# Kernel optimization log

Measured on AMD Instinct MI355X. Metric: run time of the kernel, lower is better.

Reference implementation:

```python
import jax, jax.numpy as jnp
import numpy as np

# Module config (matches init_kwargs)
H, W, C = 32, 32, 256
K = 3                      # filter_size
B = 16
TEMP = 1.0                 # softmax_temp
CH, CW = H - K + 1, W - K + 1   # convs_height/width (valid padding, stride 1)
NF = CH * CW               # num_convs
FS = K * K                 # filter_size squared (window size)
HW = H * W


def _local_indices():
    # flattened (row-major over H,W) positions of each KxK window, sorted ascending
    idx = np.zeros((NF, FS), dtype=np.int32)
    c = 0
    for i in range(CH):
        for j in range(CW):
            win = [(i + di) * W + (j + dj) for di in range(K) for dj in range(K)]
            idx[c] = np.sort(win)
            c += 1
    return jnp.asarray(idx)


def setup_inputs() -> dict:
    key = jax.random.key(0)
    ks = jax.random.split(key, 7)
    s = 1.0 / np.sqrt(C)  # torch Linear default init scale
    return {
        "batch": jax.random.normal(ks[0], (B, C, H, W), dtype=jnp.float32),
        "key_w": jax.random.uniform(ks[1], (C, C), jnp.float32, -s, s),
        "key_b": jax.random.uniform(ks[2], (C,), jnp.float32, -s, s),
        "query_w": jax.random.uniform(ks[3], (C, C), jnp.float32, -s, s),
        "query_b": jax.random.uniform(ks[4], (C,), jnp.float32, -s, s),
        "value_w": jax.random.uniform(ks[5], (1, C), jnp.float32, -s, s),
        "value_b": jax.random.uniform(ks[6], (1,), jnp.float32, -s, s),
        "local_indices": _local_indices(),
    }


def _normalize(t):
    # F.normalize(dim=-1), eps=1e-12
    return t / jnp.maximum(jnp.linalg.norm(t, axis=-1, keepdims=True), 1e-12)


def reference(batch, key_w, key_b, query_w, query_b, value_w, value_b, local_indices):
    # [B,C,H,W] -> [B,HW,C]
    x = batch.transpose(0, 2, 3, 1).reshape(B, HW, C)
    # local patches: X_l[f,b,k,c] = x[b, local_indices[f,k], c]  -> [NF,B,FS,C]
    X_l = x[:, local_indices].transpose(1, 0, 2, 3)
    # global is the full (unmasked) feature map: X_g = x  -> [B,HW,C]
    keys = x @ key_w.T + key_b                       # [B,HW,C]
    queries = X_l @ query_w.T + query_b              # [NF,B,FS,C]
    values = (x @ value_w.T + value_b)[..., 0]       # [B,HW]
    # cosine similarity: [NF,B,HW,FS]
    comp = jnp.einsum('bnc,fbkc->fbnk', _normalize(keys), _normalize(queries))
    att = jax.nn.softmax(TEMP * comp, axis=2)        # softmax over HW
    # W_g[f,b,k] = sum_n values[b,n] * att[f,b,n,k]
    W_g = jnp.einsum('bn,fbnk->fbk', values, att)
    # convolved: sum over window positions, weighted
    conv = jnp.einsum('fbk,fbkc->fbc', W_g, X_l)     # [NF,B,C]
    out = conv.transpose(1, 0, 2).reshape(B, CH, CW, C).transpose(0, 3, 1, 2)
    return out  # [B,C,CH,CW]
```

## Files before the change

kernel.cpp:

```cpp
#include <hip/hip_runtime.h>
#include <hip/hip_bf16.h>


#define NB 16
#define NC 256
#define NHW 1024
#define NCH 30

typedef __attribute__((ext_vector_type(8))) short short8;
typedef __attribute__((ext_vector_type(4))) float f32x4;

static __device__ __forceinline__ unsigned short f2bf(float f) {
    __hip_bfloat16 h = __float2bfloat16(f);
    return *(unsigned short*)&h;
}
static __device__ __forceinline__ float bf2f(unsigned short u) {
    unsigned int x = ((unsigned int)u) << 16;
    return __uint_as_float(x);
}

__global__ __launch_bounds__(256) void wconv_kernel(
    const float* __restrict__ key_w, const float* __restrict__ query_w,
    unsigned short* __restrict__ kpk, unsigned short* __restrict__ qpk)
{
    const int gx = blockIdx.x;
    const int mat = gx >> 3, g = gx & 7, t = threadIdx.x;
    const float* src = mat ? query_w : key_w;
    unsigned short* dst = mat ? qpk : kpk;
    #pragma unroll
    for (int it = 0; it < 4; ++it) {
        int idx = it * 256 + t;
        int ct = idx >> 6, lane = idx & 63;
        int l15 = lane & 15, q = lane >> 4;
        const float* s = src + (ct * 16 + l15) * NC + g * 32 + q * 8;
        float4 a = *(const float4*)s;
        float4 c = *(const float4*)(s + 4);
        short8 o;
        o[0] = (short)f2bf(a.x); o[1] = (short)f2bf(a.y);
        o[2] = (short)f2bf(a.z); o[3] = (short)f2bf(a.w);
        o[4] = (short)f2bf(c.x); o[5] = (short)f2bf(c.y);
        o[6] = (short)f2bf(c.z); o[7] = (short)f2bf(c.w);
        *(short8*)(dst + ((size_t)(g * 16 + ct) * 64 + lane) * 8) = o;
    }
}

__global__ __launch_bounds__(256, 4) void fused_lin_kernel(
    const float* __restrict__ batch,
    const float* __restrict__ value_w, const float* __restrict__ value_b,
    const unsigned short* __restrict__ kpk, const unsigned short* __restrict__ qpk,
    const float* __restrict__ key_b, const float* __restrict__ query_b,
    unsigned short* __restrict__ xc,
    unsigned short* __restrict__ Kn, unsigned short* __restrict__ Qn,
    float* __restrict__ vout)
{
    const int b = blockIdx.y, n0 = blockIdx.x * 16;
    const int t = threadIdx.x, wave = t >> 6, lane = t & 63;
    const int l15 = lane & 15, quad = lane >> 4;

    __shared__ unsigned short Xs[2][16][72];
    __shared__ float PK[4][16], PQ[4][16];
    __shared__ float4 vred[4][4];

    const int c_l = t >> 2;
    const int n4  = (t & 3) * 4;
    const float* bb = batch + (size_t)b * NC * NHW + n0;
    unsigned short* xcp = xc + (size_t)b * NC * NHW + n0;
    float4 vacc = {0.f, 0.f, 0.f, 0.f};

    const unsigned short* kbase = kpk + (size_t)(wave * 4) * 512 + lane * 8;
    const unsigned short* qbase = qpk + (size_t)(wave * 4) * 512 + lane * 8;

    short8 wK[2][4], wQ[2][4];
    #pragma unroll
    for (int ct = 0; ct < 4; ++ct) {
        wK[0][ct] = *(const short8*)(kbase + ct * 512);
        wQ[0][ct] = *(const short8*)(qbase + ct * 512);
    }

    {
        float4 x0 = *(const float4*)(bb + (size_t)c_l * NHW + n4);
        ushort4 o0;
        o0.x = f2bf(x0.x); o0.y = f2bf(x0.y); o0.z = f2bf(x0.z); o0.w = f2bf(x0.w);
        *(ushort4*)(xcp + (size_t)c_l * NHW + n4) = o0;
        float w0 = value_w[c_l];
        vacc.x += x0.x * w0; vacc.y += x0.y * w0;
        vacc.z += x0.z * w0; vacc.w += x0.w * w0;
        Xs[0][n4 + 0][c_l] = o0.x; Xs[0][n4 + 1][c_l] = o0.y;
        Xs[0][n4 + 2][c_l] = o0.z; Xs[0][n4 + 3][c_l] = o0.w;
    }
    __syncthreads();

    f32x4 accK[4], accQ[4];
    #pragma unroll
    for (int ct = 0; ct < 4; ++ct) {
        int co = wave * 64 + ct * 16 + l15;
        float bK = key_b[co], bQ = query_b[co];
        accK[ct] = (f32x4){bK, bK, bK, bK};
        accQ[ct] = (f32x4){bQ, bQ, bQ, bQ};
    }

    for (int cc = 0; cc < 4; ++cc) {
        ushort4 o0;
        if (cc < 3) {
            int c0 = (cc + 1) * 64 + c_l;
            float4 x0 = *(const float4*)(bb + (size_t)c0 * NHW + n4);
            o0.x = f2bf(x0.x); o0.y = f2bf(x0.y); o0.z = f2bf(x0.z); o0.w = f2bf(x0.w);
            *(ushort4*)(xcp + (size_t)c0 * NHW + n4) = o0;
            float w0 = value_w[c0];
            vacc.x += x0.x * w0; vacc.y += x0.y * w0;
            vacc.z += x0.z * w0; vacc.w += x0.w * w0;
        }
        const int cur = cc & 1;
        #pragma unroll
        for (int kc = 0; kc < 2; ++kc) {
            const int g = cc * 2 + kc;
            if (g < 7) {
                const int nb_ = (g + 1) & 1;
                #pragma unroll
                for (int ct = 0; ct < 4; ++ct) {
                    wK[nb_][ct] = *(const short8*)(kbase + (g + 1) * 8192 + ct * 512);
                    wQ[nb_][ct] = *(const short8*)(qbase + (g + 1) * 8192 + ct * 512);
                }
            }
            short8 af = *(const short8*)&Xs[cur][l15][kc * 32 + quad * 8];
            const int cb = g & 1;
            #pragma unroll
            for (int ct = 0; ct < 4; ++ct) {
                accK[ct] = __builtin_amdgcn_mfma_f32_16x16x32_bf16(af, wK[cb][ct], accK[ct], 0, 0, 0);
                accQ[ct] = __builtin_amdgcn_mfma_f32_16x16x32_bf16(af, wQ[cb][ct], accQ[ct], 0, 0, 0);
            }
        }
        if (cc < 3) {
            const int nxt = (cc + 1) & 1;
            Xs[nxt][n4 + 0][c_l] = o0.x; Xs[nxt][n4 + 1][c_l] = o0.y;
            Xs[nxt][n4 + 2][c_l] = o0.z; Xs[nxt][n4 + 3][c_l] = o0.w;
            __syncthreads();
        }
    }

    vacc.x += __shfl_xor(vacc.x, 4, 64); vacc.x += __shfl_xor(vacc.x, 8, 64);
    vacc.x += __shfl_xor(vacc.x, 16, 64); vacc.x += __shfl_xor(vacc.x, 32, 64);
    vacc.y += __shfl_xor(vacc.y, 4, 64); vacc.y += __shfl_xor(vacc.y, 8, 64);
    vacc.y += __shfl_xor(vacc.y, 16, 64); vacc.y += __shfl_xor(vacc.y, 32, 64);
    vacc.z += __shfl_xor(vacc.z, 4, 64); vacc.z += __shfl_xor(vacc.z, 8, 64);
    vacc.z += __shfl_xor(vacc.z, 16, 64); vacc.z += __shfl_xor(vacc.z, 32, 64);
    vacc.w += __shfl_xor(vacc.w, 4, 64); vacc.w += __shfl_xor(vacc.w, 8, 64);
    vacc.w += __shfl_xor(vacc.w, 16, 64); vacc.w += __shfl_xor(vacc.w, 32, 64);

    float nK[4] = {0, 0, 0, 0}, nQ[4] = {0, 0, 0, 0};
    #pragma unroll
    for (int ct = 0; ct < 4; ++ct)
        #pragma unroll
        for (int r = 0; r < 4; ++r) {
            nK[r] += accK[ct][r] * accK[ct][r];
            nQ[r] += accQ[ct][r] * accQ[ct][r];
        }
    #pragma unroll
    for (int r = 0; r < 4; ++r)
        #pragma unroll
        for (int o = 1; o < 16; o <<= 1) {
            nK[r] += __shfl_xor(nK[r], o, 64);
            nQ[r] += __shfl_xor(nQ[r], o, 64);
        }
    if (l15 == 0)
        #pragma unroll
        for (int r = 0; r < 4; ++r) {
            PK[wave][quad * 4 + r] = nK[r];
            PQ[wave][quad * 4 + r] = nQ[r];
        }
    if (lane < 4) vred[wave][lane] = vacc;
    __syncthreads();

    float ik[4], iq[4];
    #pragma unroll
    for (int r = 0; r < 4; ++r) {
        int qr = quad * 4 + r;
        float sk = PK[0][qr] + PK[1][qr] + PK[2][qr] + PK[3][qr];
        float sq = PQ[0][qr] + PQ[1][qr] + PQ[2][qr] + PQ[3][qr];
        ik[r] = 1.f / fmaxf(sqrtf(sk), 1e-12f);
        iq[r] = 1.f / fmaxf(sqrtf(sq), 1e-12f);
    }
    #pragma unroll
    for (int ct = 0; ct < 4; ++ct)
        #pragma unroll
        for (int r = 0; r < 4; ++r) {
            size_t row = (size_t)(b * NHW + n0 + quad * 4 + r) * NC
                       + wave * 64 + ct * 16 + l15;
            Kn[row] = f2bf(accK[ct][r] * ik[r]);
            Qn[row] = f2bf(accQ[ct][r] * iq[r]);
        }
    if (t < 4) {
        float4 s = {0.f, 0.f, 0.f, 0.f};
        #pragma unroll
        for (int w = 0; w < 4; ++w) {
            float4 p = vred[w][t];
            s.x += p.x; s.y += p.y; s.z += p.z; s.w += p.w;
        }
        float vb = value_b[0];
        s.x += vb; s.y += vb; s.z += vb; s.w += vb;
        *(float4*)(vout + b * NHW + n0 + t * 4) = s;
    }
}

__global__ __launch_bounds__(512) void attn_kernel(
    const unsigned short* __restrict__ Kn,
    const unsigned short* __restrict__ Qn,
    const float* __restrict__ vbuf,
    float* __restrict__ R)
{
    const int b = blockIdx.y, m0 = blockIdx.x * 64;
    const int t = threadIdx.x, wave = t >> 6, lane = t & 63;
    const int l15 = lane & 15, quad = lane >> 4;

    short8 bf[4][8];
    #pragma unroll
    for (int ms = 0; ms < 4; ++ms) {
        const short* q = (const short*)Qn
                       + (size_t)(b * NHW + m0 + ms * 16 + l15) * NC + quad * 8;
        #pragma unroll
        for (int c = 0; c < 8; ++c) bf[ms][c] = *(const short8*)(q + 32 * c);
    }
    const float* vb = vbuf + b * NHW;
    const int nstart = wave * 128;
    const short* ka = (const short*)Kn + (size_t)(b * NHW + nstart + l15) * NC + quad * 8;

    float z[4] = {0.f, 0.f, 0.f, 0.f}, tc[4] = {0.f, 0.f, 0.f, 0.f};
    for (int it = 0; it < 8; ++it, ka += 16 * NC) {
        short8 af[8];
        #pragma unroll
        for (int c = 0; c < 8; ++c) af[c] = *(const short8*)(ka + 32 * c);
        f32x4 a0[4], a1[4];
        #pragma unroll
        for (int ms = 0; ms < 4; ++ms) { a0[ms] = (f32x4){0,0,0,0}; a1[ms] = (f32x4){0,0,0,0}; }
        #pragma unroll
        for (int c = 0; c < 4; ++c)
            #pragma unroll
            for (int ms = 0; ms < 4; ++ms) {
                a0[ms] = __builtin_amdgcn_mfma_f32_16x16x32_bf16(af[c],     bf[ms][c],     a0[ms], 0, 0, 0);
                a1[ms] = __builtin_amdgcn_mfma_f32_16x16x32_bf16(af[c + 4], bf[ms][c + 4], a1[ms], 0, 0, 0);
            }
        float4 vv = *(const float4*)(vb + nstart + it * 16 + quad * 4);
        #pragma unroll
        for (int ms = 0; ms < 4; ++ms)
            #pragma unroll
            for (int r = 0; r < 4; ++r) {
                float e = __expf(a0[ms][r] + a1[ms][r]);
                z[ms] += e;
                tc[ms] += ((const float*)&vv)[r] * e;
            }
    }
    #pragma unroll
    for (int ms = 0; ms < 4; ++ms) {
        z[ms]  += __shfl_xor(z[ms], 16, 64);  z[ms]  += __shfl_xor(z[ms], 32, 64);
        tc[ms] += __shfl_xor(tc[ms], 16, 64); tc[ms] += __shfl_xor(tc[ms], 32, 64);
    }

    __shared__ float zs[8][4][16], ts[8][4][16];
    if (lane < 16)
        #pragma unroll
        for (int ms = 0; ms < 4; ++ms) {
            zs[wave][ms][l15] = z[ms];
            ts[wave][ms][l15] = tc[ms];
        }
    __syncthreads();
    if (t < 64) {
        int ms = t >> 4, li = t & 15;
        float zz = 0.f, tt = 0.f;
        #pragma unroll
        for (int w = 0; w < 8; ++w) { zz += zs[w][ms][li]; tt += ts[w][ms][li]; }
        R[b * NHW + m0 + ms * 16 + li] = tt / zz;
    }
}

__global__ __launch_bounds__(256) void out_kernel(
    const unsigned short* __restrict__ xc,
    const float* __restrict__ R,
    float* __restrict__ out)
{
    const int bc = blockIdx.x;
    const int b  = bc >> 8;
    const int t  = threadIdx.x;
    __shared__ float P[NHW];

    const unsigned short* xp = xc + (size_t)bc * NHW;
    const float* rp = R + b * NHW;
    {
        ushort4 xv = *(const ushort4*)(xp + t * 4);
        float4  rv = *(const float4*)(rp + t * 4);
        P[t * 4 + 0] = rv.x * bf2f(xv.x);
        P[t * 4 + 1] = rv.y * bf2f(xv.y);
        P[t * 4 + 2] = rv.z * bf2f(xv.z);
        P[t * 4 + 3] = rv.w * bf2f(xv.w);
    }
    __syncthreads();
    for (int idx = t; idx < NCH * NCH; idx += 256) {
        int i = idx / NCH, j = idx - i * NCH;
        const float* pr = &P[i * 32 + j];
        float s = pr[0]  + pr[1]  + pr[2]
                + pr[32] + pr[33] + pr[34]
                + pr[64] + pr[65] + pr[66];
        out[(size_t)bc * (NCH * NCH) + idx] = s;
    }
}

extern "C" void kernel_launch(void* const* d_in, const int* in_sizes, int n_in,
                              void* d_out, int out_size, void* d_ws, size_t ws_size,
                              hipStream_t stream) {
    const float* batch   = (const float*)d_in[0];
    const float* key_w   = (const float*)d_in[1];
    const float* key_b   = (const float*)d_in[2];
    const float* query_w = (const float*)d_in[3];
    const float* query_b = (const float*)d_in[4];
    const float* value_w = (const float*)d_in[5];
    const float* value_b = (const float*)d_in[6];
    float* out = (float*)d_out;

    char* ws = (char*)d_ws;
    const size_t KQ = (size_t)NB * NHW * NC;
    unsigned short* xc  = (unsigned short*)ws;
    unsigned short* Kn  = xc + KQ;
    unsigned short* Qn  = Kn + KQ;
    unsigned short* kpk = Qn + KQ;
    unsigned short* qpk = kpk + NC * NC;
    float* vbuf = (float*)(qpk + NC * NC);
    float* Rbuf = vbuf + NB * NHW;

    wconv_kernel<<<16, 256, 0, stream>>>(key_w, query_w, kpk, qpk);
    fused_lin_kernel<<<dim3(64, NB), 256, 0, stream>>>(batch, value_w, value_b,
                                                       kpk, qpk, key_b, query_b,
                                                       xc, Kn, Qn, vbuf);
    attn_kernel<<<dim3(16, NB), 512, 0, stream>>>(Kn, Qn, vbuf, Rbuf);
    out_kernel<<<NB * NC, 256, 0, stream>>>(xc, Rbuf, out);
}
```

Measured before the change: 132.3 us.

## Split attention over key halves and merge partial sums in output kernel

The attention kernel now processes 32 query rows per block with 4 waves, and splits the 1024 keys into two halves across a new grid dimension. Each block writes partial softmax denominators and weighted sums, and the output kernel combines the two halves before the convolution sum. This raises the block count from 256 to 1024 and lowers per-thread register use so more blocks fit on the CUs. In exchange, K rows are reloaded for twice as many query tiles, and extra partial buffers are written and read.

```diff
diff --git a/kernel.cpp b/kernel.cpp
--- a/kernel.cpp
+++ b/kernel.cpp
@@ -202,46 +202,46 @@
     }
 }
 
-__global__ __launch_bounds__(512) void attn_kernel(
+__global__ __launch_bounds__(256, 3) void attn_kernel(
     const unsigned short* __restrict__ Kn,
     const unsigned short* __restrict__ Qn,
     const float* __restrict__ vbuf,
-    float* __restrict__ R)
+    float* __restrict__ zp, float* __restrict__ tp)
 {
-    const int b = blockIdx.y, m0 = blockIdx.x * 64;
+    const int b = blockIdx.z, half = blockIdx.y, m0 = blockIdx.x * 32;
     const int t = threadIdx.x, wave = t >> 6, lane = t & 63;
     const int l15 = lane & 15, quad = lane >> 4;
 
-    short8 bf[4][8];
-    #pragma unroll
-    for (int ms = 0; ms < 4; ++ms) {
+    short8 bf[2][8];
+    #pragma unroll
+    for (int ms = 0; ms < 2; ++ms) {
         const short* q = (const short*)Qn
                        + (size_t)(b * NHW + m0 + ms * 16 + l15) * NC + quad * 8;
         #pragma unroll
         for (int c = 0; c < 8; ++c) bf[ms][c] = *(const short8*)(q + 32 * c);
     }
     const float* vb = vbuf + b * NHW;
-    const int nstart = wave * 128;
+    const int nstart = half * 512 + wave * 128;
     const short* ka = (const short*)Kn + (size_t)(b * NHW + nstart + l15) * NC + quad * 8;
 
-    float z[4] = {0.f, 0.f, 0.f, 0.f}, tc[4] = {0.f, 0.f, 0.f, 0.f};
+    float z[2] = {0.f, 0.f}, tc[2] = {0.f, 0.f};
     for (int it = 0; it < 8; ++it, ka += 16 * NC) {
         short8 af[8];
         #pragma unroll
         for (int c = 0; c < 8; ++c) af[c] = *(const short8*)(ka + 32 * c);
-        f32x4 a0[4], a1[4];
-        #pragma unroll
-        for (int ms = 0; ms < 4; ++ms) { a0[ms] = (f32x4){0,0,0,0}; a1[ms] = (f32x4){0,0,0,0}; }
+        f32x4 a0[2], a1[2];
+        #pragma unroll
+        for (int ms = 0; ms < 2; ++ms) { a0[ms] = (f32x4){0,0,0,0}; a1[ms] = (f32x4){0,0,0,0}; }
         #pragma unroll
         for (int c = 0; c < 4; ++c)
             #pragma unroll
-            for (int ms = 0; ms < 4; ++ms) {
+            for (int ms = 0; ms < 2; ++ms) {
                 a0[ms] = __builtin_amdgcn_mfma_f32_16x16x32_bf16(af[c],     bf[ms][c],     a0[ms], 0, 0, 0);
                 a1[ms] = __builtin_amdgcn_mfma_f32_16x16x32_bf16(af[c + 4], bf[ms][c + 4], a1[ms], 0, 0, 0);
             }
         float4 vv = *(const float4*)(vb + nstart + it * 16 + quad * 4);
         #pragma unroll
-        for (int ms = 0; ms < 4; ++ms)
+        for (int ms = 0; ms < 2; ++ms)
             #pragma unroll
             for (int r = 0; r < 4; ++r) {
                 float e = __expf(a0[ms][r] + a1[ms][r]);
@@ -250,31 +250,32 @@
             }
     }
     #pragma unroll
-    for (int ms = 0; ms < 4; ++ms) {
+    for (int ms = 0; ms < 2; ++ms) {
         z[ms]  += __shfl_xor(z[ms], 16, 64);  z[ms]  += __shfl_xor(z[ms], 32, 64);
         tc[ms] += __shfl_xor(tc[ms], 16, 64); tc[ms] += __shfl_xor(tc[ms], 32, 64);
     }
 
-    __shared__ float zs[8][4][16], ts[8][4][16];
+    __shared__ float zs[4][2][16], ts[4][2][16];
     if (lane < 16)
         #pragma unroll
-        for (int ms = 0; ms < 4; ++ms) {
+        for (int ms = 0; ms < 2; ++ms) {
             zs[wave][ms][l15] = z[ms];
             ts[wave][ms][l15] = tc[ms];
         }
     __syncthreads();
-    if (t < 64) {
+    if (t < 32) {
         int ms = t >> 4, li = t & 15;
         float zz = 0.f, tt = 0.f;
         #pragma unroll
-        for (int w = 0; w < 8; ++w) { zz += zs[w][ms][li]; tt += ts[w][ms][li]; }
-        R[b * NHW + m0 + ms * 16 + li] = tt / zz;
+        for (int w = 0; w < 4; ++w) { zz += zs[w][ms][li]; tt += ts[w][ms][li]; }
+        size_t o = (size_t)(half * NB + b) * NHW + m0 + ms * 16 + li;
+        zp[o] = zz; tp[o] = tt;
     }
 }
 
 __global__ __launch_bounds__(256) void out_kernel(
     const unsigned short* __restrict__ xc,
-    const float* __restrict__ R,
+    const float* __restrict__ zp, const float* __restrict__ tp,
     float* __restrict__ out)
 {
     const int bc = blockIdx.x;
@@ -283,14 +284,18 @@
     __shared__ float P[NHW];
 
     const unsigned short* xp = xc + (size_t)bc * NHW;
-    const float* rp = R + b * NHW;
     {
+        size_t o0 = (size_t)b * NHW + t * 4;
+        size_t o1 = (size_t)(NB + b) * NHW + t * 4;
+        float4 z0 = *(const float4*)(zp + o0);
+        float4 z1 = *(const float4*)(zp + o1);
+        float4 t0 = *(const float4*)(tp + o0);
+        float4 t1 = *(const float4*)(tp + o1);
         ushort4 xv = *(const ushort4*)(xp + t * 4);
-        float4  rv = *(const float4*)(rp + t * 4);
-        P[t * 4 + 0] = rv.x * bf2f(xv.x);
-        P[t * 4 + 1] = rv.y * bf2f(xv.y);
-        P[t * 4 + 2] = rv.z * bf2f(xv.z);
-        P[t * 4 + 3] = rv.w * bf2f(xv.w);
+        P[t * 4 + 0] = (t0.x + t1.x) / (z0.x + z1.x) * bf2f(xv.x);
+        P[t * 4 + 1] = (t0.y + t1.y) / (z0.y + z1.y) * bf2f(xv.y);
+        P[t * 4 + 2] = (t0.z + t1.z) / (z0.z + z1.z) * bf2f(xv.z);
+        P[t * 4 + 3] = (t0.w + t1.w) / (z0.w + z1.w) * bf2f(xv.w);
     }
     __syncthreads();
     for (int idx = t; idx < NCH * NCH; idx += 256) {
@@ -323,12 +328,13 @@
     unsigned short* kpk = Qn + KQ;
     unsigned short* qpk = kpk + NC * NC;
     float* vbuf = (float*)(qpk + NC * NC);
-    float* Rbuf = vbuf + NB * NHW;
+    float* zbuf = vbuf + NB * NHW;
+    float* tbuf = zbuf + 2 * NB * NHW;
 
     wconv_kernel<<<16, 256, 0, stream>>>(key_w, query_w, kpk, qpk);
     fused_lin_kernel<<<dim3(64, NB), 256, 0, stream>>>(batch, value_w, value_b,
                                                        kpk, qpk, key_b, query_b,
                                                        xc, Kn, Qn, vbuf);
-    attn_kernel<<<dim3(16, NB), 512, 0, stream>>>(Kn, Qn, vbuf, Rbuf);
-    out_kernel<<<NB * NC, 256, 0, stream>>>(xc, Rbuf, out);
-}
+    attn_kernel<<<dim3(32, 2, NB), 256, 0, stream>>>(Kn, Qn, vbuf, zbuf, tbuf);
+    out_kernel<<<NB * NC, 256, 0, stream>>>(xc, zbuf, tbuf, out);
+}
```

Measured after the change: 145.5 us. +10.0%, slower.
